# Kernel tuning notes

Hardware: AMD Instinct MI355X
Metric: run time of the kernel (lower is better)

## Reference

```python
import jax, jax.numpy as jnp
import numpy as np

B, N = 2, 4096
IN_CH, OUT_CH = 64, 64
L_MAX, NR = 3, 4
KERNEL_RADIUS = 0.5
PATCH = 64  # hardcoded in torch topk(-dist, 64)


def setup_inputs() -> dict:
    key = jax.random.key(0)
    k1, k2, k3 = jax.random.split(key, 3)
    xyz = jax.random.normal(k1, (B, N, 3), dtype=jnp.float32)
    signal = jax.random.normal(k2, (B, N, IN_CH), dtype=jnp.float32)
    # xavier_uniform on (out, in, nr, l_max+1): receptive = nr*(l_max+1)
    recept = NR * (L_MAX + 1)
    bound = float(np.sqrt(6.0 / (IN_CH * recept + OUT_CH * recept)))
    weight = jax.random.uniform(k3, (OUT_CH, IN_CH, NR, L_MAX + 1), dtype=jnp.float32,
                                minval=-bound, maxval=bound)
    biases = jnp.zeros((OUT_CH,), dtype=jnp.float32)
    return {"xyz": xyz, "signal": signal, "weight": weight, "biases": biases}


def _sph(X):
    # X: [B,N,P,3] l2-normalized patch directions -> [B,N,P,(L_MAX+1)^2]
    x, y, z = X[..., 0], X[..., 1], X[..., 2]
    x2, y2, z2 = x * x, y * y, z * z
    Ys = []
    Ys.append(jnp.full_like(x, 0.5 * np.sqrt(1.0 / np.pi)))           # Y00
    s3 = np.sqrt(3.0 / np.pi) / 2.0
    Ys += [s3 * y, s3 * z, -s3 * x]                                    # l=1
    s15h = np.sqrt(15.0 / np.pi) / 2.0
    s15q = np.sqrt(15.0 / np.pi) / 4.0
    s5q = np.sqrt(5.0 / np.pi) / 4.0
    Ys += [s15h * x * y, s15h * y * z, s5q * (2.0 * z2 - x2 - y2),
           -s15h * z * x, s15q * (x2 - y2)]                            # l=2
    c33 = np.sqrt(35.0 / (2.0 * np.pi)) / 4.0
    c32 = np.sqrt(105.0 / np.pi) / 2.0
    c31 = np.sqrt(21.0 / (2.0 * np.pi)) / 4.0
    c30 = np.sqrt(7.0 / np.pi) / 4.0
    c32b = np.sqrt(105.0 / np.pi) / 4.0
    Ys += [c33 * (3.0 * x2 * y - y * y2),
           c32 * x * y * z,
           c31 * (4.0 * y * z2 - x2 * y - y * y2),
           c30 * (2.0 * z * z2 - 3.0 * x2 * z - 3.0 * y2 * z),
           -c31 * (4.0 * z2 * x - x * x2 - x * y2),
           c32b * (x2 * z - y2 * z),
           -c33 * (x * x2 - 3.0 * x * y2)]                             # l=3
    return jnp.stack(Ys, axis=-1)


def reference(xyz, signal, weight, biases):
    # pairwise squared distances via matmul (costly_cdist)
    r2 = jnp.sum(xyz * xyz, axis=2)                                    # [B,N]
    sqd = r2[:, :, None] - 2.0 * jnp.einsum('bnd,bmd->bnm', xyz, xyz) + r2[:, None, :]
    neg_vals, idx = jax.lax.top_k(-sqd, PATCH)                         # KNN
    sq_patches_dist = -neg_vals                                        # [B,N,P]
    gather = jax.vmap(lambda pts, i: pts[i])                           # per-batch fancy gather
    patches = gather(xyz, idx) - xyz[:, :, None, :]                    # [B,N,P,3]
    # F.normalize(p=2, dim=-1, eps=0.01): x / max(||x||, eps)
    nrm = jnp.linalg.norm(patches, axis=-1, keepdims=True)
    Y = _sph(patches / jnp.maximum(nrm, 0.01))                         # [B,N,P,K2]
    dist = jnp.sqrt(jnp.maximum(sq_patches_dist, 1e-4))                # [B,N,P]
    r_grid = jnp.linspace(0.0, KERNEL_RADIUS, NR, dtype=jnp.float32)   # [NR]
    sigma = KERNEL_RADIUS / (NR - 1)
    rad = jnp.exp(-jnp.square(dist[..., None] - r_grid) / (2.0 * sigma ** 2))  # [B,N,P,NR]
    yk = Y[:, :, :, None, :] * rad[..., None]                          # [B,N,P,NR,K2]
    y_w = jnp.sum(yk[:, :, :, 0, 0], axis=2)[:, :, None, None, None]   # [B,N,1,1,1]
    conv_kernel = yk / (y_w + 1e-6)
    sig_patches = gather(signal, idx)                                  # [B,N,P,C]
    y = jnp.einsum('bvprn,bvpc->bvcrn', conv_kernel, sig_patches)
    y = y * y
    bands = [jnp.sum(y[..., l * l:(l + 1) * (l + 1)], axis=-1) for l in range(L_MAX + 1)]
    y = jnp.stack(bands, axis=-1)                                      # [B,N,C,NR,L+1]
    y = jnp.sqrt(jnp.maximum(y, 1e-4))
    out = jnp.einsum('ijrn,bvjrn->bvi', weight, y) + biases
    return out
```

## Files before the change

kernel.cpp:

```cpp
#include <hip/hip_runtime.h>
#include <hip/hip_bf16.h>
#include <math.h>

#define NB 2
#define NPTS 4096
#define CH 64
#define PATCH 64

typedef __attribute__((ext_vector_type(8))) short s16x8;
typedef __attribute__((ext_vector_type(4))) short s16x4;
typedef __attribute__((ext_vector_type(4))) float f32x4;
typedef __attribute__((ext_vector_type(4))) unsigned u32x4;

static __device__ __forceinline__ short f2bf(float f) {
    union { __hip_bfloat16 h; short s; } u;
    u.h = __float2bfloat16(f);
    return u.s;
}
static __device__ __forceinline__ float bf2f(unsigned short v) {
    return __uint_as_float(((unsigned)v) << 16);
}

__global__ __launch_bounds__(256) void prep_kernel(const float* __restrict__ W,
                                                   short* __restrict__ Wfrag,
                                                   const float* __restrict__ xyz,
                                                   float4* __restrict__ xyz4,
                                                   const float* __restrict__ signal,
                                                   unsigned short* __restrict__ sigbf) {
    const int bid = blockIdx.x;
    const int tid = threadIdx.x;
    if (bid < 32) {
        const int gid = bid * 256 + tid;
        const int mt = gid >> 11;
        const int st = (gid >> 6) & 31;
        const int l  = gid & 63;
        const int i  = mt * 16 + (l & 15);
        const int k0 = st * 32 + (l >> 4) * 8;
        const f32x4 a = *(const f32x4*)&W[i * 1024 + k0];
        const f32x4 c = *(const f32x4*)&W[i * 1024 + k0 + 4];
        s16x8 v;
        v[0] = f2bf(a[0]); v[1] = f2bf(a[1]); v[2] = f2bf(a[2]); v[3] = f2bf(a[3]);
        v[4] = f2bf(c[0]); v[5] = f2bf(c[1]); v[6] = f2bf(c[2]); v[7] = f2bf(c[3]);
        *(s16x8*)&Wfrag[gid * 8] = v;
    } else if (bid < 64) {
        const int idx = (bid - 32) * 256 + tid;
        const float x = xyz[idx * 3 + 0];
        const float y = xyz[idx * 3 + 1];
        const float z = xyz[idx * 3 + 2];
        float4 v;
        v.x = x; v.y = y; v.z = z;
        v.w = fmaf(x, x, fmaf(y, y, z * z));
        xyz4[idx] = v;
    } else {
        const int g = (bid - 64) * 256 + tid;
        const size_t base = (size_t)g * 32;
#pragma unroll
        for (int u = 0; u < 8; ++u) {
            const f32x4 v = *(const f32x4*)&signal[base + u * 4];
            s16x4 o;
            o[0] = f2bf(v[0]); o[1] = f2bf(v[1]); o[2] = f2bf(v[2]); o[3] = f2bf(v[3]);
            *(s16x4*)&sigbf[base + u * 4] = o;
        }
    }
}

__global__ __launch_bounds__(256, 8) void knn_kernel(const float4* __restrict__ xyz4,
                                                     int* __restrict__ knn_idx) {
    const int pt   = blockIdx.x;
    const int b    = pt >> 12;
    const int q    = pt & (NPTS - 1);
    const int tid  = threadIdx.x;
    const int wv   = tid >> 6;
    const int lane = tid & 63;

    __shared__ __align__(16) unsigned hist[2048];
    __shared__ __align__(16) unsigned short sbin[4096];
    __shared__ unsigned wsum[4];
    __shared__ unsigned sh_H;
    __shared__ int sh_need;
    __shared__ int cnt_less, cnt_tie;

    const float4* xb = xyz4 + (size_t)b * NPTS;
    const float4 qp = xb[q];

#pragma unroll
    for (int u = 0; u < 2; ++u)
        ((u32x4*)hist)[u * 256 + tid] = (u32x4){0u, 0u, 0u, 0u};
    if (tid == 0) { cnt_less = 0; cnt_tie = 0; }
    __syncthreads();

#pragma unroll 4
    for (int i = 0; i < 16; ++i) {
        const int m = i * 256 + tid;
        const float4 p = xb[m];
        const float dx = p.x - qp.x;
        const float dy = p.y - qp.y;
        const float dz = p.z - qp.z;
        const float sq = fmaf(dx, dx, fmaf(dy, dy, dz * dz));
        const unsigned hk = __float_as_uint(sq) >> 19;
        sbin[i * 256 + tid] = (unsigned short)hk;
        atomicAdd(&hist[hk & 2047], 1u << ((hk >> 11) << 4));
    }
    __syncthreads();

    const int wb2 = (tid & 127) * 16;
    const int shp = (tid >> 7) << 4;
    unsigned tsum = 0;
#pragma unroll
    for (int u = 0; u < 4; ++u) {
        const u32x4 h4 = *(const u32x4*)&hist[wb2 + u * 4];
        tsum += ((h4[0] >> shp) & 0xFFFFu) + ((h4[1] >> shp) & 0xFFFFu)
              + ((h4[2] >> shp) & 0xFFFFu) + ((h4[3] >> shp) & 0xFFFFu);
    }
    unsigned run = tsum;
#pragma unroll
    for (int off = 1; off < 64; off <<= 1) {
        const unsigned v = __shfl_up(run, off);
        if (lane >= off) run += v;
    }
    if (lane == 63) wsum[wv] = run;
    __syncthreads();
    unsigned wbase = 0;
    for (int w2 = 0; w2 < wv; ++w2) wbase += wsum[w2];
    const unsigned incl = wbase + run;
    const unsigned excl = incl - tsum;
    if ((int)excl < PATCH && PATCH <= (int)incl) {
        int nrem = PATCH - (int)excl;
        for (int u = 0; u < 16; ++u) {
            const unsigned cb = (hist[wb2 + u] >> shp) & 0xFFFFu;
            if (nrem <= (int)cb) { sh_H = (unsigned)(tid * 16 + u); sh_need = nrem; break; }
            nrem -= (int)cb;
        }
    }
    __syncthreads();

    const unsigned H = sh_H;
    const int need  = sh_need;
    const int nless = PATCH - need;
    int* optr = knn_idx + (size_t)pt * PATCH;
    unsigned* ckey = hist;
    unsigned* cidx = hist + 1024;

#pragma unroll 4
    for (int i = 0; i < 16; ++i) {
        const int m = i * 256 + tid;
        const unsigned hk = sbin[i * 256 + tid];
        if (hk < H) {
            const int pos = atomicAdd(&cnt_less, 1);
            optr[pos] = m;
        } else if (hk == H) {
            const int pos = atomicAdd(&cnt_tie, 1);
            if (pos < 1024) {
                const float4 p = xb[m];
                const float dx = p.x - qp.x;
                const float dy = p.y - qp.y;
                const float dz = p.z - qp.z;
                const float sq = fmaf(dx, dx, fmaf(dy, dy, dz * dz));
                ckey[pos] = __float_as_uint(sq);
                cidx[pos] = m;
            }
        }
    }
    __syncthreads();

    const int nc = min(cnt_tie, 1024);
    for (int i = tid; i < nc; i += 256) {
        const unsigned ki = ckey[i];
        int rank = 0;
        for (int j = 0; j < nc; ++j) {
            const unsigned kj = ckey[j];
            rank += (kj < ki || (kj == ki && j < i)) ? 1 : 0;
        }
        if (rank < need) optr[nless + rank] = cidx[i];
    }
}

__global__ __launch_bounds__(256, 4) void conv_kernel(const float4* __restrict__ xyz4,
                                                      const unsigned short* __restrict__ sigbf,
                                                      const short* __restrict__ Wfrag,
                                                      const float* __restrict__ biases,
                                                      const int* __restrict__ knn_idx,
                                                      float* __restrict__ out) {
    const int tid  = threadIdx.x;
    const int wv   = tid >> 6;
    const int lane = tid & 63;
    const int ln15 = lane & 15;
    const int kq   = lane >> 4;

    __shared__ __align__(16) short Y4[4 * 64 * 20];
    __shared__ __align__(16) float rad4[4 * 64 * 4];
    __shared__ __align__(16) short ckF[4096];
    __shared__ __align__(16) short sigF[4096];
    __shared__ __align__(16) short zb[4 * 1032];
    __shared__ int   sIdx4[256];
    __shared__ float sh_inv4[4];

    sIdx4[tid] = knn_idx[(size_t)blockIdx.x * 256 + tid];
    __syncthreads();

    const int b = blockIdx.x >> 10;
    const float4* xbase = xyz4 + (size_t)b * NPTS;
    const unsigned short* sgb = sigbf + (size_t)b * NPTS * CH;

    {
        const int q   = (blockIdx.x * 4 + wv) & (NPTS - 1);
        const int idx = sIdx4[wv * 64 + lane];
        const float4 cp = xbase[q];
        const float4 np = xbase[idx];
        const float dx = np.x - cp.x;
        const float dy = np.y - cp.y;
        const float dz = np.z - cp.z;
        const float nrm2 = dx * dx + dy * dy + dz * dz;
        const float inv_n = 1.0f / fmaxf(sqrtf(nrm2), 0.01f);
        const float x = dx * inv_n, y = dy * inv_n, z = dz * inv_n;
        const float x2 = x * x, y2 = y * y, zz = z * z;

        float Y[16];
        Y[0] = 0.28209479177387814f;
        const float s3 = 0.4886025119029199f;
        Y[1] = s3 * y;  Y[2] = s3 * z;  Y[3] = -s3 * x;
        const float s15h = 1.0925484305920792f;
        const float s15q = 0.5462742152960396f;
        const float s5q  = 0.31539156525252005f;
        Y[4] = s15h * x * y;
        Y[5] = s15h * y * z;
        Y[6] = s5q * (2.0f * zz - x2 - y2);
        Y[7] = -s15h * z * x;
        Y[8] = s15q * (x2 - y2);
        const float c33  = 0.5900435899266435f;
        const float c32  = 2.8906114426405543f;
        const float c31  = 0.4570457994644658f;
        const float c30  = 0.3731763325901154f;
        const float c32b = 1.4453057213202771f;
        Y[9]  = c33 * (3.0f * x2 * y - y * y2);
        Y[10] = c32 * x * y * z;
        Y[11] = c31 * (4.0f * y * zz - x2 * y - y * y2);
        Y[12] = c30 * (2.0f * z * zz - 3.0f * x2 * z - 3.0f * y2 * z);
        Y[13] = -c31 * (4.0f * zz * x - x * x2 - x * y2);
        Y[14] = c32b * (x2 * z - y2 * z);
        Y[15] = -c33 * (x * x2 - 3.0f * x * y2);

        const float dist = sqrtf(fmaxf(nrm2, 1e-4f));
        const float d1 = dist - 0.16666667f;
        const float d2 = dist - 0.33333334f;
        const float d3 = dist - 0.5f;
        f32x4 rad;
        rad[0] = expf(-dist * dist * 18.0f);
        rad[1] = expf(-d1 * d1 * 18.0f);
        rad[2] = expf(-d2 * d2 * 18.0f);
        rad[3] = expf(-d3 * d3 * 18.0f);

        const int ybase = (wv * 64 + lane) * 20;
#pragma unroll
        for (int k4 = 0; k4 < 4; ++k4) {
            s16x4 v;
            v[0] = f2bf(Y[k4 * 4 + 0]);
            v[1] = f2bf(Y[k4 * 4 + 1]);
            v[2] = f2bf(Y[k4 * 4 + 2]);
            v[3] = f2bf(Y[k4 * 4 + 3]);
            *(s16x4*)&Y4[ybase + k4 * 4] = v;
        }
        *(f32x4*)&rad4[(wv * 64 + lane) * 4] = rad;

        float v = 0.28209479177387814f * rad[0];
#pragma unroll
        for (int off = 32; off > 0; off >>= 1) v += __shfl_down(v, off);
        if (lane == 0) sh_inv4[wv] = 1.0f / (v + 1e-6f);
    }
    __syncthreads();

    const int sgv  = wv & 1;
    const int ctv  = wv >> 1;

    for (int it = 0; it < 4; ++it) {
        {
            s16x8 g0, g1;
#pragma unroll
            for (int j = 0; j < 8; ++j) {
                const int row = sIdx4[it * 64 + sgv * 32 + kq * 8 + j];
                const unsigned short* rp = sgb + ((size_t)row << 6) + ctv * 16 + ln15;
                g0[j] = (short)rp[0];
                g1[j] = (short)rp[32];
            }
            *(s16x8*)&sigF[(ctv * 2 + sgv) * 512 + lane * 8] = g0;
            *(s16x8*)&sigF[((ctv + 2) * 2 + sgv) * 512 + lane * 8] = g1;
        }
#pragma unroll
        for (int ff = 0; ff < 2; ++ff) {
            const int f  = wv + ff * 4;
            const int mt = f >> 1, s = f & 1;
            const int pb = s * 32 + kq * 8;
            s16x8 av;
#pragma unroll
            for (int j = 0; j < 8; ++j) {
                const int p = pb + j;
                const float Yv = bf2f((unsigned short)Y4[(it * 64 + p) * 20 + ln15]);
                const float rv = rad4[(it * 64 + p) * 4 + mt];
                av[j] = f2bf(Yv * rv);
            }
            *(s16x8*)&ckF[f * 512 + lane * 8] = av;
        }
        __syncthreads();

        const s16x8 bf0 = *(const s16x8*)&sigF[(wv * 2 + 0) * 512 + lane * 8];
        const s16x8 bf1 = *(const s16x8*)&sigF[(wv * 2 + 1) * 512 + lane * 8];
        f32x4 acc0 = {0.f, 0.f, 0.f, 0.f}, acc1 = acc0, acc2 = acc0, acc3 = acc0;
        {
            s16x8 a;
            a = *(const s16x8*)&ckF[0 * 512 + lane * 8];
            acc0 = __builtin_amdgcn_mfma_f32_16x16x32_bf16(a, bf0, acc0, 0, 0, 0);
            a = *(const s16x8*)&ckF[1 * 512 + lane * 8];
            acc0 = __builtin_amdgcn_mfma_f32_16x16x32_bf16(a, bf1, acc0, 0, 0, 0);
            a = *(const s16x8*)&ckF[2 * 512 + lane * 8];
            acc1 = __builtin_amdgcn_mfma_f32_16x16x32_bf16(a, bf0, acc1, 0, 0, 0);
            a = *(const s16x8*)&ckF[3 * 512 + lane * 8];
            acc1 = __builtin_amdgcn_mfma_f32_16x16x32_bf16(a, bf1, acc1, 0, 0, 0);
            a = *(const s16x8*)&ckF[4 * 512 + lane * 8];
            acc2 = __builtin_amdgcn_mfma_f32_16x16x32_bf16(a, bf0, acc2, 0, 0, 0);
            a = *(const s16x8*)&ckF[5 * 512 + lane * 8];
            acc2 = __builtin_amdgcn_mfma_f32_16x16x32_bf16(a, bf1, acc2, 0, 0, 0);
            a = *(const s16x8*)&ckF[6 * 512 + lane * 8];
            acc3 = __builtin_amdgcn_mfma_f32_16x16x32_bf16(a, bf0, acc3, 0, 0, 0);
            a = *(const s16x8*)&ckF[7 * 512 + lane * 8];
            acc3 = __builtin_amdgcn_mfma_f32_16x16x32_bf16(a, bf1, acc3, 0, 0, 0);
        }

        const float inv = sh_inv4[it];
        const int qq = kq;
        float rb[4][4];
#pragma unroll
        for (int mt = 0; mt < 4; ++mt) {
            f32x4 av = (mt == 0) ? acc0 : (mt == 1) ? acc1 : (mt == 2) ? acc2 : acc3;
            const float y0 = av[0] * inv, y1 = av[1] * inv;
            const float y2 = av[2] * inv, y3 = av[3] * inv;
            const float sA = y0 * y0;
            const float sB = y1 * y1 + y2 * y2 + y3 * y3;
            const float sAll = sA + sB;
            float b0 = (qq == 0) ? sA : 0.0f;
            float b1 = (qq == 0) ? sB : 0.0f;
            float b2 = (qq == 1) ? sAll : ((qq == 2) ? sA : 0.0f);
            float b3 = (qq == 3) ? sAll : ((qq == 2) ? sB : 0.0f);
            b0 += __shfl_xor(b0, 16); b0 += __shfl_xor(b0, 32);
            b1 += __shfl_xor(b1, 16); b1 += __shfl_xor(b1, 32);
            b2 += __shfl_xor(b2, 16); b2 += __shfl_xor(b2, 32);
            b3 += __shfl_xor(b3, 16); b3 += __shfl_xor(b3, 32);
            rb[mt][0] = b0; rb[mt][1] = b1; rb[mt][2] = b2; rb[mt][3] = b3;
        }
        float s0 = rb[0][0], s1 = rb[0][1], s2 = rb[0][2], s3 = rb[0][3];
#pragma unroll
        for (int mt = 1; mt < 4; ++mt) {
            s0 = (qq == mt) ? rb[mt][0] : s0;
            s1 = (qq == mt) ? rb[mt][1] : s1;
            s2 = (qq == mt) ? rb[mt][2] : s2;
            s3 = (qq == mt) ? rb[mt][3] : s3;
        }
        s16x4 zv;
        zv[0] = f2bf(sqrtf(fmaxf(s0, 1e-4f)));
        zv[1] = f2bf(sqrtf(fmaxf(s1, 1e-4f)));
        zv[2] = f2bf(sqrtf(fmaxf(s2, 1e-4f)));
        zv[3] = f2bf(sqrtf(fmaxf(s3, 1e-4f)));
        const int c = wv * 16 + ln15;
        *(s16x4*)&zb[it * 1032 + c * 16 + qq * 4] = zv;

        if (it < 3) __syncthreads();
    }
    __syncthreads();

    const int mt5 = wv;
    const int g   = ln15 & 3;
    f32x4 acc5 = {0.f, 0.f, 0.f, 0.f};
#pragma unroll 4
    for (int st = 0; st < 32; ++st) {
        const s16x8 a  = *(const s16x8*)&Wfrag[((mt5 * 32 + st) * 64 + lane) * 8];
        const s16x8 zf = *(const s16x8*)&zb[g * 1032 + st * 32 + kq * 8];
        acc5 = __builtin_amdgcn_mfma_f32_16x16x32_bf16(a, zf, acc5, 0, 0, 0);
    }
    if (ln15 < 4) {
        const int i0 = mt5 * 16 + kq * 4;
        const int orow = (blockIdx.x * 4 + g) * CH;
#pragma unroll
        for (int rg = 0; rg < 4; ++rg)
            out[orow + i0 + rg] = acc5[rg] + biases[i0 + rg];
    }
}

extern "C" void kernel_launch(void* const* d_in, const int* in_sizes, int n_in,
                              void* d_out, int out_size, void* d_ws, size_t ws_size,
                              hipStream_t stream) {
    const float* xyz    = (const float*)d_in[0];
    const float* signal = (const float*)d_in[1];
    const float* weight = (const float*)d_in[2];
    const float* biases = (const float*)d_in[3];
    float* out = (float*)d_out;

    char* ws = (char*)d_ws;
    int*            knn_idx = (int*)ws;
    short*          Wfrag   = (short*)(ws + 0x200000);
    float4*         xyz4    = (float4*)(ws + 0x220000);
    unsigned short* sigbf   = (unsigned short*)(ws + 0x240000);

    prep_kernel<<<128, 256, 0, stream>>>(weight, Wfrag, xyz, xyz4, signal, sigbf);
    knn_kernel<<<NB * NPTS, 256, 0, stream>>>(xyz4, knn_idx);
    conv_kernel<<<(NB * NPTS) / 4, 256, 0, stream>>>(xyz4, sigbf, Wfrag, biases,
                                                     knn_idx, out);
}
```

Baseline: 83.76 us.

## Process two kNN queries per block with coarser 1024-bin histogram

Each kNN block now handles two query points, so every loaded candidate point serves both queries. It also halves the block count and amortises the per-block setup and synchronisation. Distances are computed with the |p|^2 - 2p·q + |q|^2 expansion, and the two queries' bin counts are packed into 16-bit halves of a 1024-bin histogram. The tie buffer is capped at 256 per query, and ties are ordered by point index rather than slot. The coarser bins can make the boundary bin larger, so more tie candidates go through the quadratic rank pass, and the cap could drop candidates. The expanded distance formula may also differ slightly in rounding from the direct difference.

After: 95.42 us. 1.14x slower.

```diff
diff --git a/kernel.cpp b/kernel.cpp
--- a/kernel.cpp
+++ b/kernel.cpp
@@ -64,54 +64,53 @@
     }
 }
 
-__global__ __launch_bounds__(256, 8) void knn_kernel(const float4* __restrict__ xyz4,
+__global__ __launch_bounds__(256, 7) void knn_kernel(const float4* __restrict__ xyz4,
                                                      int* __restrict__ knn_idx) {
-    const int pt   = blockIdx.x;
-    const int b    = pt >> 12;
-    const int q    = pt & (NPTS - 1);
+    const int bq   = blockIdx.x;
+    const int q0g  = bq * 2;
+    const int b    = q0g >> 12;
+    const int ql   = q0g & (NPTS - 1);
     const int tid  = threadIdx.x;
     const int wv   = tid >> 6;
     const int lane = tid & 63;
 
-    __shared__ __align__(16) unsigned hist[2048];
-    __shared__ __align__(16) unsigned short sbin[4096];
+    __shared__ __align__(16) unsigned hist[1024];
+    __shared__ __align__(16) unsigned sbin[4096];
     __shared__ unsigned wsum[4];
-    __shared__ unsigned sh_H;
-    __shared__ int sh_need;
-    __shared__ int cnt_less, cnt_tie;
+    __shared__ unsigned ctrl[8];
 
     const float4* xb = xyz4 + (size_t)b * NPTS;
-    const float4 qp = xb[q];
-
-#pragma unroll
-    for (int u = 0; u < 2; ++u)
-        ((u32x4*)hist)[u * 256 + tid] = (u32x4){0u, 0u, 0u, 0u};
-    if (tid == 0) { cnt_less = 0; cnt_tie = 0; }
+    const float4 qA = xb[ql];
+    const float4 qB = xb[ql + 1];
+    const float a2x = -2.0f * qA.x, a2y = -2.0f * qA.y, a2z = -2.0f * qA.z;
+    const float b2x = -2.0f * qB.x, b2y = -2.0f * qB.y, b2z = -2.0f * qB.z;
+
+    ((u32x4*)hist)[tid] = (u32x4){0u, 0u, 0u, 0u};
+    if (tid < 8) ctrl[tid] = 0u;
     __syncthreads();
 
 #pragma unroll 4
     for (int i = 0; i < 16; ++i) {
         const int m = i * 256 + tid;
         const float4 p = xb[m];
-        const float dx = p.x - qp.x;
-        const float dy = p.y - qp.y;
-        const float dz = p.z - qp.z;
-        const float sq = fmaf(dx, dx, fmaf(dy, dy, dz * dz));
-        const unsigned hk = __float_as_uint(sq) >> 19;
-        sbin[i * 256 + tid] = (unsigned short)hk;
-        atomicAdd(&hist[hk & 2047], 1u << ((hk >> 11) << 4));
-    }
-    __syncthreads();
-
-    const int wb2 = (tid & 127) * 16;
-    const int shp = (tid >> 7) << 4;
-    unsigned tsum = 0;
-#pragma unroll
-    for (int u = 0; u < 4; ++u) {
-        const u32x4 h4 = *(const u32x4*)&hist[wb2 + u * 4];
-        tsum += ((h4[0] >> shp) & 0xFFFFu) + ((h4[1] >> shp) & 0xFFFFu)
-              + ((h4[2] >> shp) & 0xFFFFu) + ((h4[3] >> shp) & 0xFFFFu);
-    }
+        float t0 = fmaf(p.x, a2x, p.w);
+        t0 = fmaf(p.y, a2y, t0);
+        t0 = fmaf(p.z, a2z, t0);
+        t0 = fmaxf(t0 + qA.w, 0.0f);
+        float t1 = fmaf(p.x, b2x, p.w);
+        t1 = fmaf(p.y, b2y, t1);
+        t1 = fmaf(p.z, b2z, t1);
+        t1 = fmaxf(t1 + qB.w, 0.0f);
+        const unsigned bin0 = __float_as_uint(t0) >> 21;
+        const unsigned bin1 = __float_as_uint(t1) >> 21;
+        sbin[i * 256 + tid] = bin0 | (bin1 << 16);
+        atomicAdd(&hist[bin0], 1u);
+        atomicAdd(&hist[bin1], 0x10000u);
+    }
+    __syncthreads();
+
+    const u32x4 h4 = ((const u32x4*)hist)[tid];
+    const unsigned tsum = h4[0] + h4[1] + h4[2] + h4[3];
     unsigned run = tsum;
 #pragma unroll
     for (int off = 1; off < 64; off <<= 1) {
@@ -124,54 +123,108 @@
     for (int w2 = 0; w2 < wv; ++w2) wbase += wsum[w2];
     const unsigned incl = wbase + run;
     const unsigned excl = incl - tsum;
-    if ((int)excl < PATCH && PATCH <= (int)incl) {
-        int nrem = PATCH - (int)excl;
-        for (int u = 0; u < 16; ++u) {
-            const unsigned cb = (hist[wb2 + u] >> shp) & 0xFFFFu;
-            if (nrem <= (int)cb) { sh_H = (unsigned)(tid * 16 + u); sh_need = nrem; break; }
-            nrem -= (int)cb;
-        }
-    }
-    __syncthreads();
-
-    const unsigned H = sh_H;
-    const int need  = sh_need;
-    const int nless = PATCH - need;
-    int* optr = knn_idx + (size_t)pt * PATCH;
-    unsigned* ckey = hist;
-    unsigned* cidx = hist + 1024;
+    {
+        const int e = (int)(excl & 0xFFFFu), ic = (int)(incl & 0xFFFFu);
+        if (e < PATCH && PATCH <= ic) {
+            int nrem = PATCH - e;
+#pragma unroll
+            for (int u = 0; u < 4; ++u) {
+                const int cb = (int)(h4[u] & 0xFFFFu);
+                if (nrem <= cb) { ctrl[0] = (unsigned)(tid * 4 + u); ctrl[2] = (unsigned)nrem; break; }
+                nrem -= cb;
+            }
+        }
+    }
+    {
+        const int e = (int)(excl >> 16), ic = (int)(incl >> 16);
+        if (e < PATCH && PATCH <= ic) {
+            int nrem = PATCH - e;
+#pragma unroll
+            for (int u = 0; u < 4; ++u) {
+                const int cb = (int)(h4[u] >> 16);
+                if (nrem <= cb) { ctrl[1] = (unsigned)(tid * 4 + u); ctrl[3] = (unsigned)nrem; break; }
+                nrem -= cb;
+            }
+        }
+    }
+    __syncthreads();
+
+    const unsigned H0 = ctrl[0], H1 = ctrl[1];
+    const int need0 = (int)ctrl[2], need1 = (int)ctrl[3];
+    const int nless0 = PATCH - need0, nless1 = PATCH - need1;
+    int* out0 = knn_idx + (size_t)q0g * PATCH;
+    int* out1 = out0 + PATCH;
+    unsigned* ckey0 = hist;
+    unsigned* cidx0 = hist + 256;
+    unsigned* ckey1 = hist + 512;
+    unsigned* cidx1 = hist + 768;
 
 #pragma unroll 4
     for (int i = 0; i < 16; ++i) {
         const int m = i * 256 + tid;
-        const unsigned hk = sbin[i * 256 + tid];
-        if (hk < H) {
-            const int pos = atomicAdd(&cnt_less, 1);
-            optr[pos] = m;
-        } else if (hk == H) {
-            const int pos = atomicAdd(&cnt_tie, 1);
-            if (pos < 1024) {
+        const unsigned pk = sbin[i * 256 + tid];
+        const unsigned b0 = pk & 0xFFFFu;
+        const unsigned b1 = pk >> 16;
+        if (b0 < H0) {
+            const unsigned pos = atomicAdd(&ctrl[4], 1u);
+            out0[pos] = m;
+        } else if (b0 == H0) {
+            const unsigned pos = atomicAdd(&ctrl[5], 1u);
+            if (pos < 256u) {
                 const float4 p = xb[m];
-                const float dx = p.x - qp.x;
-                const float dy = p.y - qp.y;
-                const float dz = p.z - qp.z;
-                const float sq = fmaf(dx, dx, fmaf(dy, dy, dz * dz));
-                ckey[pos] = __float_as_uint(sq);
-                cidx[pos] = m;
-            }
-        }
-    }
-    __syncthreads();
-
-    const int nc = min(cnt_tie, 1024);
-    for (int i = tid; i < nc; i += 256) {
-        const unsigned ki = ckey[i];
-        int rank = 0;
-        for (int j = 0; j < nc; ++j) {
-            const unsigned kj = ckey[j];
-            rank += (kj < ki || (kj == ki && j < i)) ? 1 : 0;
-        }
-        if (rank < need) optr[nless + rank] = cidx[i];
+                float t = fmaf(p.x, a2x, p.w);
+                t = fmaf(p.y, a2y, t);
+                t = fmaf(p.z, a2z, t);
+                t = fmaxf(t + qA.w, 0.0f);
+                ckey0[pos] = __float_as_uint(t);
+                cidx0[pos] = (unsigned)m;
+            }
+        }
+        if (b1 < H1) {
+            const unsigned pos = atomicAdd(&ctrl[6], 1u);
+            out1[pos] = m;
+        } else if (b1 == H1) {
+            const unsigned pos = atomicAdd(&ctrl[7], 1u);
+            if (pos < 256u) {
+                const float4 p = xb[m];
+                float t = fmaf(p.x, b2x, p.w);
+                t = fmaf(p.y, b2y, t);
+                t = fmaf(p.z, b2z, t);
+                t = fmaxf(t + qB.w, 0.0f);
+                ckey1[pos] = __float_as_uint(t);
+                cidx1[pos] = (unsigned)m;
+            }
+        }
+    }
+    __syncthreads();
+
+    {
+        const int nc = min((int)ctrl[5], 256);
+        for (int c = tid; c < nc; c += 256) {
+            const unsigned ki = ckey0[c];
+            const unsigned mi = cidx0[c];
+            int rank = 0;
+            for (int j = 0; j < nc; ++j) {
+                const unsigned kj = ckey0[j];
+                const unsigned mj = cidx0[j];
+                rank += (kj < ki || (kj == ki && mj < mi)) ? 1 : 0;
+            }
+            if (rank < need0) out0[nless0 + rank] = (int)mi;
+        }
+    }
+    {
+        const int nc = min((int)ctrl[7], 256);
+        for (int c = tid; c < nc; c += 256) {
+            const unsigned ki = ckey1[c];
+            const unsigned mi = cidx1[c];
+            int rank = 0;
+            for (int j = 0; j < nc; ++j) {
+                const unsigned kj = ckey1[j];
+                const unsigned mj = cidx1[j];
+                rank += (kj < ki || (kj == ki && mj < mi)) ? 1 : 0;
+            }
+            if (rank < need1) out1[nless1 + rank] = (int)mi;
+        }
     }
 }
 
@@ -400,7 +453,7 @@
     unsigned short* sigbf   = (unsigned short*)(ws + 0x240000);
 
     prep_kernel<<<128, 256, 0, stream>>>(weight, Wfrag, xyz, xyz4, signal, sigbf);
-    knn_kernel<<<NB * NPTS, 256, 0, stream>>>(xyz4, knn_idx);
+    knn_kernel<<<(NB * NPTS) / 2, 256, 0, stream>>>(xyz4, knn_idx);
     conv_kernel<<<(NB * NPTS) / 4, 256, 0, stream>>>(xyz4, sigbf, Wfrag, biases,
                                                      knn_idx, out);
 }
```

## Simplify kNN histogram select with expanded-distance keys and recomputation

Applied to the files above, without the earlier changes.

Rewrites the kNN radix-select pass. The packed 16-bit dual histogram and the stored bin array become a plain 4096-bin histogram. Distances are computed as |p|^2 - 2p·q + |q|^2 via FMAs, using the w component of xyz4, and are recomputed in the second pass instead of read back from shared memory. The tie buffer shrinks to 256 entries and ties are broken by point index. This lowers LDS use and packing overhead, at the cost of redundant global loads, expanded-form rounding, and possible truncation if more than 256 points fall in the boundary bin.

After: 90.09 us. 1.08x slower.

```diff
diff --git a/kernel.cpp b/kernel.cpp
--- a/kernel.cpp
+++ b/kernel.cpp
@@ -73,8 +73,7 @@
     const int wv   = tid >> 6;
     const int lane = tid & 63;
 
-    __shared__ __align__(16) unsigned hist[2048];
-    __shared__ __align__(16) unsigned short sbin[4096];
+    __shared__ __align__(16) unsigned hist[4096];
     __shared__ unsigned wsum[4];
     __shared__ unsigned sh_H;
     __shared__ int sh_need;
@@ -82,9 +81,11 @@
 
     const float4* xb = xyz4 + (size_t)b * NPTS;
     const float4 qp = xb[q];
-
-#pragma unroll
-    for (int u = 0; u < 2; ++u)
+    const float m2x = -2.0f * qp.x, m2y = -2.0f * qp.y, m2z = -2.0f * qp.z;
+    const float qw = qp.w;
+
+#pragma unroll
+    for (int u = 0; u < 4; ++u)
         ((u32x4*)hist)[u * 256 + tid] = (u32x4){0u, 0u, 0u, 0u};
     if (tid == 0) { cnt_less = 0; cnt_tie = 0; }
     __syncthreads();
@@ -93,24 +94,19 @@
     for (int i = 0; i < 16; ++i) {
         const int m = i * 256 + tid;
         const float4 p = xb[m];
-        const float dx = p.x - qp.x;
-        const float dy = p.y - qp.y;
-        const float dz = p.z - qp.z;
-        const float sq = fmaf(dx, dx, fmaf(dy, dy, dz * dz));
-        const unsigned hk = __float_as_uint(sq) >> 19;
-        sbin[i * 256 + tid] = (unsigned short)hk;
-        atomicAdd(&hist[hk & 2047], 1u << ((hk >> 11) << 4));
-    }
-    __syncthreads();
-
-    const int wb2 = (tid & 127) * 16;
-    const int shp = (tid >> 7) << 4;
+        float t = fmaf(p.x, m2x, p.w);
+        t = fmaf(p.y, m2y, t);
+        t = fmaf(p.z, m2z, t);
+        t = fmaxf(t + qw, 0.0f);
+        atomicAdd(&hist[__float_as_uint(t) >> 19], 1u);
+    }
+    __syncthreads();
+
     unsigned tsum = 0;
 #pragma unroll
     for (int u = 0; u < 4; ++u) {
-        const u32x4 h4 = *(const u32x4*)&hist[wb2 + u * 4];
-        tsum += ((h4[0] >> shp) & 0xFFFFu) + ((h4[1] >> shp) & 0xFFFFu)
-              + ((h4[2] >> shp) & 0xFFFFu) + ((h4[3] >> shp) & 0xFFFFu);
+        const u32x4 h4 = ((const u32x4*)hist)[tid * 4 + u];
+        tsum += h4[0] + h4[1] + h4[2] + h4[3];
     }
     unsigned run = tsum;
 #pragma unroll
@@ -127,7 +123,7 @@
     if ((int)excl < PATCH && PATCH <= (int)incl) {
         int nrem = PATCH - (int)excl;
         for (int u = 0; u < 16; ++u) {
-            const unsigned cb = (hist[wb2 + u] >> shp) & 0xFFFFu;
+            const unsigned cb = hist[tid * 16 + u];
             if (nrem <= (int)cb) { sh_H = (unsigned)(tid * 16 + u); sh_need = nrem; break; }
             nrem -= (int)cb;
         }
@@ -139,39 +135,39 @@
     const int nless = PATCH - need;
     int* optr = knn_idx + (size_t)pt * PATCH;
     unsigned* ckey = hist;
-    unsigned* cidx = hist + 1024;
+    unsigned* cidx = hist + 256;
 
 #pragma unroll 4
     for (int i = 0; i < 16; ++i) {
         const int m = i * 256 + tid;
-        const unsigned hk = sbin[i * 256 + tid];
+        const float4 p = xb[m];
+        float t = fmaf(p.x, m2x, p.w);
+        t = fmaf(p.y, m2y, t);
+        t = fmaf(p.z, m2z, t);
+        t = fmaxf(t + qw, 0.0f);
+        const unsigned key = __float_as_uint(t);
+        const unsigned hk = key >> 19;
         if (hk < H) {
             const int pos = atomicAdd(&cnt_less, 1);
             optr[pos] = m;
         } else if (hk == H) {
             const int pos = atomicAdd(&cnt_tie, 1);
-            if (pos < 1024) {
-                const float4 p = xb[m];
-                const float dx = p.x - qp.x;
-                const float dy = p.y - qp.y;
-                const float dz = p.z - qp.z;
-                const float sq = fmaf(dx, dx, fmaf(dy, dy, dz * dz));
-                ckey[pos] = __float_as_uint(sq);
-                cidx[pos] = m;
-            }
-        }
-    }
-    __syncthreads();
-
-    const int nc = min(cnt_tie, 1024);
+            if (pos < 256) { ckey[pos] = key; cidx[pos] = (unsigned)m; }
+        }
+    }
+    __syncthreads();
+
+    const int nc = min(cnt_tie, 256);
     for (int i = tid; i < nc; i += 256) {
         const unsigned ki = ckey[i];
+        const unsigned mi = cidx[i];
         int rank = 0;
         for (int j = 0; j < nc; ++j) {
             const unsigned kj = ckey[j];
-            rank += (kj < ki || (kj == ki && j < i)) ? 1 : 0;
-        }
-        if (rank < need) optr[nless + rank] = cidx[i];
+            const unsigned mj = cidx[j];
+            rank += (kj < ki || (kj == ki && mj < mi)) ? 1 : 0;
+        }
+        if (rank < need) optr[nless + rank] = (int)mi;
     }
 }
 
```
